# Kernel tuning notes

Hardware: AMD Instinct MI355X
Metric: run time of the kernel (lower is better)

The kernel has to match this reference:

```python
import jax, jax.numpy as jnp
import numpy as np

BS, NQ, NPTS, VOC, MAXLEN, NGT, EDIM = 16, 100, 25, 96, 25, 32, 300
ALPHA, GAMMA = 0.25, 2.0
CLASS_W, COORD_W, TEXT_W = 1.0, 1.0, 1.0
EPS_KL = 1e-6


def setup_inputs() -> dict:
    key = jax.random.key(0)
    ks = jax.random.split(key, 6)
    return {
        "pred_logits": jax.random.normal(ks[0], (BS, NQ, NPTS, 1), jnp.float32),
        "pred_ctrl_points": jax.random.uniform(ks[1], (BS, NQ, NPTS, 2), dtype=jnp.float32),
        "pred_text_logits": jax.random.normal(ks[2], (BS, NQ, NPTS, VOC + 1), jnp.float32),
        "tgt_ctrl_points": jax.random.uniform(ks[3], (BS, NGT, NPTS, 2), dtype=jnp.float32),
        "target_texts": jax.random.randint(ks[4], (BS, NGT, MAXLEN), 0, VOC + 1).astype(jnp.int32),
        "centroids": jax.random.normal(ks[5], (VOC, EDIM), jnp.float32),
    }


def reference(pred_logits, pred_ctrl_points, pred_text_logits, tgt_ctrl_points, target_texts, centroids):
    bs, nq = pred_logits.shape[:2]
    ngt = tgt_ctrl_points.shape[1]
    voc = centroids.shape[0]

    # ---- focal classification cost (per query, class 0) ----
    prob = jax.nn.sigmoid(pred_logits).reshape(bs * nq, NPTS, -1).mean(axis=1)  # (bs*nq, 1)
    neg = (1.0 - ALPHA) * prob ** GAMMA * -jnp.log(1.0 - prob + 1e-8)
    pos = ALPHA * (1.0 - prob) ** GAMMA * -jnp.log(prob + 1e-8)
    cost_class = (pos - neg)[:, 0]  # (bs*nq,)

    # ---- L1 cdist on flattened control points ----
    out_pts = pred_ctrl_points.reshape(bs * nq, -1)   # (bs*nq, npts*2)
    tgt_pts = tgt_ctrl_points.reshape(bs * ngt, -1)   # (bs*ngt, npts*2)
    cost_kpts = jnp.sum(jnp.abs(out_pts[:, None, :] - tgt_pts[None, :, :]), axis=-1)  # (bs*nq, bs*ngt)

    # ---- batched pairwise linguistic (KL) cost ----
    text_prob = jax.nn.softmax(pred_text_logits, axis=-1)[..., :voc]  # (bs,nq,npts,voc)
    pred_avg = text_prob.mean(axis=2)                                  # (bs,nq,voc)

    mask = (target_texts != voc)                 # padding index == voc
    lengths = mask.sum(axis=-1)                  # (bs,ngt)
    safe_idx = jnp.clip(target_texts, 0, voc - 1)
    # soft target per character: softmax over centroid similarities (generate_soft_target_sequence)
    sim = centroids[safe_idx] @ centroids.T / jnp.sqrt(jnp.float32(EDIM))  # (bs,ngt,maxlen,voc)
    char_dist = jax.nn.softmax(sim, axis=-1)
    tgt_avg = jnp.sum(char_dist * mask[..., None], axis=2) / jnp.maximum(lengths, 1)[..., None]  # (bs,ngt,voc)

    pred_s = jnp.maximum(pred_avg, EPS_KL)       # clamp(min=eps)
    tgt_s = jnp.maximum(tgt_avg, EPS_KL)
    tgt_s = tgt_s / tgt_s.sum(axis=-1, keepdims=True)
    logp = jnp.log(pred_s)                       # (bs,nq,voc)
    neg_ent = jnp.sum(tgt_s * jnp.log(tgt_s), axis=-1)  # (bs,ngt)
    kl = neg_ent[:, None, :] - jnp.einsum('bqc,bgc->bqg', logp, tgt_s)  # (bs,nq,ngt)
    kl = jnp.maximum(kl, 0.0)
    kl = jnp.where(lengths[:, None, :] == 0, 100.0, kl)

    # scatter per-image text cost into block-diagonal (bs*nq, bs*ngt)
    idx = jnp.arange(bs)
    cost_text = jnp.zeros((bs, nq, bs, ngt), pred_avg.dtype)
    cost_text = cost_text.at[idx, :, idx, :].set(kl)
    cost_text = cost_text.reshape(bs * nq, bs * ngt)

    C = CLASS_W * cost_class[:, None] + COORD_W * cost_kpts + TEXT_W * cost_text
    return C.reshape(bs, nq, bs * ngt)
```

## Files before the change

### kernel.cpp

```cpp
#include <hip/hip_runtime.h>
#include <math.h>

#define BS 16
#define NQ 100
#define NPTS 25
#define VOC 96
#define NC 97
#define MAXLEN 25
#define NGT 32
#define EDIM 300
#define NCOL 512
#define NDIM 50

#define WS_GRAM 0
#define WS_LOGP (WS_GRAM + NC * VOC)
#define WS_CC   (WS_LOGP + 1600 * VOC)
#define WS_TGTT (WS_CC + 1600)
#define WS_STAT (WS_TGTT + NDIM * NCOL)

#define GRAM_BLKS VOC
#define PRED_BLKS 1600
#define TR_BLKS 200
#define K1_BLKS (GRAM_BLKS + PRED_BLKS + TR_BLKS)

__global__ __launch_bounds__(128) void k1_kernel(
        const float* __restrict__ logits1,
        const float* __restrict__ tlogits,
        const float* __restrict__ cen,
        const float* __restrict__ tgt_pts,
        float* __restrict__ gram, float* __restrict__ logp,
        float* __restrict__ cost_class, float* __restrict__ tgtT) {
    __shared__ float smem[448];
    int blk = blockIdx.x, tid = threadIdx.x;
    int wave = tid >> 6, lane = tid & 63;

    if (blk < GRAM_BLKS) {
        float* row = smem;
        float* red = smem + 320;
        for (int k = tid; k < EDIM; k += 128) row[k] = cen[blk * EDIM + k];
        if (blk == 0 && tid < VOC) gram[VOC * VOC + tid] = 0.f;
        __syncthreads();
        float e = 0.f;
        if (tid < VOC) {
            float a0 = 0.f, a1 = 0.f;
            const float* c = cen + (size_t)tid * EDIM;
            for (int k = 0; k < EDIM; k += 2) { a0 += row[k] * c[k]; a1 += row[k + 1] * c[k + 1]; }
            e = __expf((a0 + a1) * 0.05773502691896258f);
        }
        red[tid] = e;
        __syncthreads();
        for (int s = 64; s; s >>= 1) { if (tid < s) red[tid] += red[tid + s]; __syncthreads(); }
        if (tid < VOC) gram[blk * VOC + tid] = e / red[0];
    } else if (blk < GRAM_BLKS + PRED_BLKS) {
        int u = blk - GRAM_BLKS;
        const float* base = tlogits + (size_t)u * NPTS * NC;
        float e0[13], e1[13], s[13], vm[13];
        int p0 = wave * 13;
#pragma unroll
        for (int i = 0; i < 13; ++i) {
            int p = p0 + i;
            bool ok = p < NPTS;
            vm[i] = ok ? 1.f : 0.f;
            int pe = ok ? p : 0;
            float x0 = base[pe * NC + lane];
            float x1 = (lane < 33) ? base[pe * NC + 64 + lane] : 0.f;
            e0[i] = __expf(x0);
            e1[i] = (lane < 33) ? __expf(x1) : 0.f;
            s[i] = e0[i] + e1[i];
        }
#pragma unroll
        for (int st = 32; st; st >>= 1) {
#pragma unroll
            for (int i = 0; i < 13; ++i) s[i] += __shfl_xor(s[i], st);
        }
        float part0 = 0.f, part1 = 0.f;
#pragma unroll
        for (int i = 0; i < 13; ++i) {
            float rinv = vm[i] / s[i];
            part0 += e0[i] * rinv;
            part1 += e1[i] * rinv;
        }
        float* pA = smem;
        pA[wave * 97 + lane] = part0;
        if (lane < 33) pA[wave * 97 + 64 + lane] = part1;
        __syncthreads();
        if (tid < VOC) {
            float tot = (pA[tid] + pA[97 + tid]) * 0.04f;
            logp[(size_t)u * VOC + tid] = __logf(fmaxf(tot, 1e-6f));
        }
        if (wave == 1) {
            float sig = 0.f;
            if (lane < NPTS) { float x = logits1[u * NPTS + lane]; sig = 1.f / (1.f + __expf(-x)); }
#pragma unroll
            for (int o = 32; o; o >>= 1) sig += __shfl_xor(sig, o);
            if (lane == 0) {
                float prob = sig * 0.04f;
                float negc = 0.75f * prob * prob * (-__logf(1.f - prob + 1e-8f));
                float posc = 0.25f * (1.f - prob) * (1.f - prob) * (-__logf(prob + 1e-8f));
                cost_class[u] = posc - negc;
            }
        }
    } else {
        int g = (blk - GRAM_BLKS - PRED_BLKS) * 128 + tid;
        int k = g / NCOL;
        int j = g - k * NCOL;
        tgtT[g] = tgt_pts[(size_t)j * NDIM + k];
    }
}

__global__ __launch_bounds__(256) void stats_kernel(
        const int*   __restrict__ texts,
        const float* __restrict__ gram,
        float* __restrict__ stat) {
    __shared__ int s_tex[4 * MAXLEN];
    int blk = blockIdx.x, tid = threadIdx.x;
    int wave = tid >> 6, lane = tid & 63;
    if (tid < 4 * MAXLEN) s_tex[tid] = texts[blk * 4 * MAXLEN + tid];
    __syncthreads();

    int vv[MAXLEN];
#pragma unroll
    for (int l = 0; l < MAXLEN; ++l) vv[l] = s_tex[wave * MAXLEN + l];
    int len = 0;
#pragma unroll
    for (int l = 0; l < MAXLEN; ++l) len += (vv[l] != VOC);
    float a0 = 0.f, a1 = 0.f;
#pragma unroll
    for (int l0 = 0; l0 < MAXLEN; l0 += 5) {
        float b0[5], b1[5];
#pragma unroll
        for (int q = 0; q < 5; ++q) {
            const float* gr = gram + vv[l0 + q] * VOC;
            b0[q] = gr[lane];
            b1[q] = (lane < 32) ? gr[64 + lane] : 0.f;
        }
#pragma unroll
        for (int q = 0; q < 5; ++q) { a0 += b0[q]; a1 += b1[q]; }
    }
    float dinv = 1.f / (float)(len > 0 ? len : 1);
    float t0 = fmaxf(a0 * dinv, 1e-6f);
    float t1 = (lane < 32) ? fmaxf(a1 * dinv, 1e-6f) : 0.f;
    float s = t0 + t1;
#pragma unroll
    for (int o = 32; o; o >>= 1) s += __shfl_xor(s, o);
    float inv = 1.f / s;
    float ts0 = t0 * inv, ts1 = t1 * inv;
    float c0 = ts0 * __logf(ts0);
    float c1 = (lane < 32) ? ts1 * __logf(ts1) : 0.f;
    float ent = c0 + c1;
#pragma unroll
    for (int o = 32; o; o >>= 1) ent += __shfl_xor(ent, o);
    float* dst = stat + (size_t)(blk * 4 + wave) * NC;
    dst[lane] = len ? ts0 : 0.f;
    if (lane < 32) dst[64 + lane] = len ? ts1 : 0.f;
    if (lane == 0) dst[VOC] = len ? ent : 100.f;
}

__global__ __launch_bounds__(256) void asm_kernel(
        const float* __restrict__ pred_pts,
        const float* __restrict__ tgtT,
        const float* __restrict__ logp,
        const float* __restrict__ cc,
        const float* __restrict__ stat,
        float* __restrict__ out) {
    __shared__ float s_stat[NGT * NC];
    __shared__ float s_lp[2][VOC];
    __shared__ float s_pp[2][NDIM];
    __shared__ float s_ct[2][NGT];
    __shared__ float spart[256];
    __shared__ float s_cc[2];

    int blk = blockIdx.x, tid = threadIdx.x;
    int r0 = blk * 2;
    int b = blk / 50;

    for (int i = tid; i < NGT * NC; i += 256) s_stat[i] = stat[(size_t)b * NGT * NC + i];
    if (tid < 2 * VOC) { int r = tid >= VOC, c = tid - r * VOC; s_lp[r][c] = logp[(size_t)(r0 + r) * VOC + c]; }
    if (tid < 2 * NDIM) { int r = tid >= NDIM, k = tid - r * NDIM; s_pp[r][k] = pred_pts[(size_t)(r0 + r) * NDIM + k]; }
    if (tid < 2) s_cc[tid] = cc[r0 + tid];
    __syncthreads();

    {
        int pair = tid >> 2, sub = tid & 3;
        int row = pair >> 5, g = pair & 31;
        const float* L = s_lp[row] + sub * 24;
        const float* S = s_stat + g * NC + sub * 24;
        float d0 = 0.f, d1 = 0.f;
#pragma unroll
        for (int j = 0; j < 24; j += 2) { d0 += L[j] * S[j]; d1 += L[j + 1] * S[j + 1]; }
        spart[tid] = d0 + d1;
    }
    __syncthreads();
    if (tid < 2 * NGT) {
        int row = tid >> 5, g = tid & 31;
        float s = spart[tid * 4] + spart[tid * 4 + 1] + spart[tid * 4 + 2] + spart[tid * 4 + 3];
        s_ct[row][g] = fmaxf(s_stat[g * NC + VOC] - s, 0.f);
    }

    float a00 = 0.f, a01 = 0.f, a10 = 0.f, a11 = 0.f;
#pragma unroll 10
    for (int k = 0; k < NDIM; ++k) {
        float tv0 = tgtT[(k << 9) + tid];
        float tv1 = tgtT[(k << 9) + 256 + tid];
        float p0 = s_pp[0][k], p1 = s_pp[1][k];
        a00 += fabsf(p0 - tv0);
        a01 += fabsf(p0 - tv1);
        a10 += fabsf(p1 - tv0);
        a11 += fabsf(p1 - tv1);
    }
    __syncthreads();

    int gb = tid >> 5, g = tid & 31;
    float c0v = s_cc[0], c1v = s_cc[1];
    float m0 = (gb == b) ? 1.f : 0.f;
    float m1 = (8 + gb == b) ? 1.f : 0.f;
    out[(size_t)r0 * NCOL + tid]             = c0v + a00 + m0 * s_ct[0][g];
    out[(size_t)r0 * NCOL + 256 + tid]       = c0v + a01 + m1 * s_ct[0][g];
    out[(size_t)(r0 + 1) * NCOL + tid]       = c1v + a10 + m0 * s_ct[1][g];
    out[(size_t)(r0 + 1) * NCOL + 256 + tid] = c1v + a11 + m1 * s_ct[1][g];
}

extern "C" void kernel_launch(void* const* d_in, const int* in_sizes, int n_in,
                              void* d_out, int out_size, void* d_ws, size_t ws_size,
                              hipStream_t stream) {
    const float* pred_logits      = (const float*)d_in[0];
    const float* pred_ctrl_points = (const float*)d_in[1];
    const float* pred_text_logits = (const float*)d_in[2];
    const float* tgt_ctrl_points  = (const float*)d_in[3];
    const int*   target_texts     = (const int*)d_in[4];
    const float* centroids        = (const float*)d_in[5];
    float* out = (float*)d_out;
    float* ws  = (float*)d_ws;

    float* gram = ws + WS_GRAM;
    float* logp = ws + WS_LOGP;
    float* cc   = ws + WS_CC;
    float* tgtT = ws + WS_TGTT;
    float* stat = ws + WS_STAT;

    k1_kernel<<<K1_BLKS, 128, 0, stream>>>(pred_logits, pred_text_logits, centroids,
                                           tgt_ctrl_points, gram, logp, cc, tgtT);
    stats_kernel<<<128, 256, 0, stream>>>(target_texts, gram, stat);
    asm_kernel<<<800, 256, 0, stream>>>(pred_ctrl_points, tgtT, logp, cc, stat, out);
}
```

Measured before the change: 28.41 us.

## Split assembly kernel by column half and skip text cost off-diagonal

The assembly kernel now launches twice as many blocks, and each block covers one 256-column half of the output for two query rows. Only the block whose half holds the image's own block-diagonal computes the KL text cost, so the other half skips the logp load and the dot products. The stat table is read straight from global memory instead of being staged in shared memory. This removes redundant staging and text work and raises parallelism. In exchange, pred points and class cost are loaded twice, and the stat reads are strided uncached global accesses.

```diff
diff --git a/kernel.cpp b/kernel.cpp
--- a/kernel.cpp
+++ b/kernel.cpp
@@ -163,7 +163,6 @@
         const float* __restrict__ cc,
         const float* __restrict__ stat,
         float* __restrict__ out) {
-    __shared__ float s_stat[NGT * NC];
     __shared__ float s_lp[2][VOC];
     __shared__ float s_pp[2][NDIM];
     __shared__ float s_ct[2][NGT];
@@ -171,53 +170,56 @@
     __shared__ float s_cc[2];
 
     int blk = blockIdx.x, tid = threadIdx.x;
-    int r0 = blk * 2;
-    int b = blk / 50;
-
-    for (int i = tid; i < NGT * NC; i += 256) s_stat[i] = stat[(size_t)b * NGT * NC + i];
-    if (tid < 2 * VOC) { int r = tid >= VOC, c = tid - r * VOC; s_lp[r][c] = logp[(size_t)(r0 + r) * VOC + c]; }
+    int pairIdx = blk >> 1, half = blk & 1;
+    int r0 = pairIdx * 2;
+    int b = pairIdx / 50;
+    int col0 = half << 8;
+    bool hasText = ((b >> 3) == half);
+
     if (tid < 2 * NDIM) { int r = tid >= NDIM, k = tid - r * NDIM; s_pp[r][k] = pred_pts[(size_t)(r0 + r) * NDIM + k]; }
     if (tid < 2) s_cc[tid] = cc[r0 + tid];
+    if (hasText && tid >= 64 && tid < 64 + 2 * VOC) {
+        int t = tid - 64;
+        int r = t >= VOC, c = t - r * VOC;
+        s_lp[r][c] = logp[(size_t)(r0 + r) * VOC + c];
+    }
     __syncthreads();
 
-    {
-        int pair = tid >> 2, sub = tid & 3;
-        int row = pair >> 5, g = pair & 31;
-        const float* L = s_lp[row] + sub * 24;
-        const float* S = s_stat + g * NC + sub * 24;
-        float d0 = 0.f, d1 = 0.f;
-#pragma unroll
-        for (int j = 0; j < 24; j += 2) { d0 += L[j] * S[j]; d1 += L[j + 1] * S[j + 1]; }
-        spart[tid] = d0 + d1;
-    }
-    __syncthreads();
-    if (tid < 2 * NGT) {
-        int row = tid >> 5, g = tid & 31;
-        float s = spart[tid * 4] + spart[tid * 4 + 1] + spart[tid * 4 + 2] + spart[tid * 4 + 3];
-        s_ct[row][g] = fmaxf(s_stat[g * NC + VOC] - s, 0.f);
-    }
-
-    float a00 = 0.f, a01 = 0.f, a10 = 0.f, a11 = 0.f;
+    if (hasText) {
+        {
+            int pair = tid >> 2, sub = tid & 3;
+            int row = pair >> 5, g = pair & 31;
+            const float* L = s_lp[row] + sub * 24;
+            const float* S = stat + (size_t)(b * NGT + g) * NC + sub * 24;
+            float d0 = 0.f, d1 = 0.f;
+#pragma unroll
+            for (int j = 0; j < 24; j += 2) { d0 += L[j] * S[j]; d1 += L[j + 1] * S[j + 1]; }
+            spart[tid] = d0 + d1;
+        }
+        __syncthreads();
+        if (tid < 2 * NGT) {
+            int row = tid >> 5, g = tid & 31;
+            float s = spart[tid * 4] + spart[tid * 4 + 1] + spart[tid * 4 + 2] + spart[tid * 4 + 3];
+            s_ct[row][g] = fmaxf(stat[(size_t)(b * NGT + g) * NC + VOC] - s, 0.f);
+        }
+    }
+
+    float a0 = 0.f, a1 = 0.f;
 #pragma unroll 10
     for (int k = 0; k < NDIM; ++k) {
-        float tv0 = tgtT[(k << 9) + tid];
-        float tv1 = tgtT[(k << 9) + 256 + tid];
-        float p0 = s_pp[0][k], p1 = s_pp[1][k];
-        a00 += fabsf(p0 - tv0);
-        a01 += fabsf(p0 - tv1);
-        a10 += fabsf(p1 - tv0);
-        a11 += fabsf(p1 - tv1);
+        float tv = tgtT[(k << 9) + col0 + tid];
+        a0 += fabsf(s_pp[0][k] - tv);
+        a1 += fabsf(s_pp[1][k] - tv);
     }
     __syncthreads();
 
     int gb = tid >> 5, g = tid & 31;
+    float m = (hasText && gb == (b & 7)) ? 1.f : 0.f;
     float c0v = s_cc[0], c1v = s_cc[1];
-    float m0 = (gb == b) ? 1.f : 0.f;
-    float m1 = (8 + gb == b) ? 1.f : 0.f;
-    out[(size_t)r0 * NCOL + tid]             = c0v + a00 + m0 * s_ct[0][g];
-    out[(size_t)r0 * NCOL + 256 + tid]       = c0v + a01 + m1 * s_ct[0][g];
-    out[(size_t)(r0 + 1) * NCOL + tid]       = c1v + a10 + m0 * s_ct[1][g];
-    out[(size_t)(r0 + 1) * NCOL + 256 + tid] = c1v + a11 + m1 * s_ct[1][g];
+    float t0 = m * (hasText ? s_ct[0][g] : 0.f);
+    float t1 = m * (hasText ? s_ct[1][g] : 0.f);
+    out[(size_t)r0 * NCOL + col0 + tid]       = c0v + a0 + t0;
+    out[(size_t)(r0 + 1) * NCOL + col0 + tid] = c1v + a1 + t1;
 }
 
 extern "C" void kernel_launch(void* const* d_in, const int* in_sizes, int n_in,
@@ -241,5 +243,5 @@
     k1_kernel<<<K1_BLKS, 128, 0, stream>>>(pred_logits, pred_text_logits, centroids,
                                            tgt_ctrl_points, gram, logp, cc, tgtT);
     stats_kernel<<<128, 256, 0, stream>>>(target_texts, gram, stat);
-    asm_kernel<<<800, 256, 0, stream>>>(pred_ctrl_points, tgtT, logp, cc, stat, out);
-}
+    asm_kernel<<<1600, 256, 0, stream>>>(pred_ctrl_points, tgtT, logp, cc, stat, out);
+}
```

Result: faster. 25.14 us (-11.5%).
